# Kernel tuning notes

Hardware: AMD Instinct MI355X
Metric: run time of the kernel (lower is better)

The kernel has to match this reference:

```python
import jax, jax.numpy as jnp
import numpy as np

NS, NI, NC, C, E, M = 50000, 20000, 1000, 128, 1000000, 250000


def setup_inputs() -> dict:
    key = jax.random.key(0)
    ks = jax.random.split(key, 12)
    xavier = (2.0 / (C + C)) ** 0.5  # xavier_normal_ std for square weight
    return {
        "stu_x": jax.random.normal(ks[0], (NS, C), jnp.float32),
        "item_x": jax.random.normal(ks[1], (NI, C), jnp.float32),
        "conc_x": jax.random.normal(ks[2], (NC, C), jnp.float32),
        "W_stu": jax.random.normal(ks[3], (C, C), jnp.float32) * xavier,
        "b_stu": jnp.zeros((C,), jnp.float32),
        "W_item": jax.random.normal(ks[4], (C, C), jnp.float32) * xavier,
        "b_item": jnp.zeros((C,), jnp.float32),
        "W_pred": jax.random.normal(ks[5], (1, C), jnp.float32) * ((2.0 / (1 + C)) ** 0.5),
        "b_pred": jnp.zeros((1,), jnp.float32),
        "stu_track": jax.random.randint(ks[6], (E,), 0, NS, jnp.int32),
        "item_index": jax.random.randint(ks[7], (E,), 0, NI, jnp.int32),
        "conc_index": jax.random.randint(ks[8], (E,), 0, NC, jnp.int32),
        "mean_index": jax.random.randint(ks[9], (E,), 0, M, jnp.int32),
        "num_segments": M,
    }


def _segment_mean(vals, seg_ids, num_segments):
    sums = jax.ops.segment_sum(vals, seg_ids, num_segments=num_segments)
    cnt = jax.ops.segment_sum(jnp.ones((vals.shape[0], 1), vals.dtype), seg_ids,
                              num_segments=num_segments)
    return sums / jnp.maximum(cnt, 1.0)


def reference(stu_x, item_x, conc_x, W_stu, b_stu, W_item, b_item, W_pred, b_pred,
              stu_track, item_index, conc_index, mean_index, num_segments):
    # Feature (stu): shared lin_l=lin_r; aggregate is identity -> per-edge output
    conc_s = conc_x @ W_stu.T          # [NC, C] projected source (concepts)
    stu_p = stu_x @ W_stu.T            # [NS, C] projected target (students)
    stu_feature = jax.nn.sigmoid(conc_s[conc_index] + stu_p[stu_track] + b_stu)  # [E, C]

    # Feature (item): SparseTensor(row=item, col=conc) -> x_j from conc, x_i from item
    conc_i = conc_x @ W_item.T         # [NC, C]
    item_p = item_x @ W_item.T         # [NI, C]
    item_feature = jax.nn.sigmoid(conc_i[conc_index] + item_p[item_index] + b_item)  # [E, C]

    # scatter-mean of per-edge difference over mean_index groups
    pred_input = _segment_mean(stu_feature - item_feature, mean_index, num_segments)  # [M, C]
    pred = jax.nn.sigmoid(pred_input @ W_pred.T + b_pred)  # [M, 1]
    return pred.reshape(-1)
```

## Files before the change

### kernel.cpp

```cpp
#include <hip/hip_runtime.h>

typedef unsigned short u16;
typedef unsigned int   u32;

typedef short short8 __attribute__((ext_vector_type(8)));
typedef float floatx4 __attribute__((ext_vector_type(4)));

#define CDIM 128
#define K_NEG_LOG2E -1.4426950408889634f

__device__ __forceinline__ float bf2f_lo(u32 h) {
    union { u32 u; float f; } v; v.u = h << 16; return v.f;
}
__device__ __forceinline__ float bf2f_hi(u32 h) {
    union { u32 u; float f; } v; v.u = h & 0xffff0000u; return v.f;
}
__device__ __forceinline__ u16 f2bf(float f) {
    union { float f; u32 u; } v; v.f = f;
    u32 u = v.u;
    return (u16)((u + 0x7FFFu + ((u >> 16) & 1u)) >> 16);
}
__device__ __forceinline__ float sig_pre(float y) {
    return __builtin_amdgcn_rcpf(1.0f + __builtin_amdgcn_exp2f(y));
}
__device__ __forceinline__ float sig_std(float x) {
    return __builtin_amdgcn_rcpf(1.0f + __builtin_amdgcn_exp2f(x * K_NEG_LOG2E));
}

__global__ __launch_bounds__(256) void prep_kernel(
    const float* __restrict__ Wstu, const float* __restrict__ Witem,
    u32* __restrict__ Wbf_pair, float4* __restrict__ zero4, int nZero4)
{
    const int tid = blockIdx.x * blockDim.x + threadIdx.x;
    const int stride = gridDim.x * blockDim.x;
    for (int i = tid; i < 16384; i += stride) {
        const float* W = (i & 8192) ? (Witem - 16384) : Wstu;
        const int j = i * 2;
        u32 lo = f2bf(W[j]     * K_NEG_LOG2E);
        u32 hi = f2bf(W[j + 1] * K_NEG_LOG2E);
        Wbf_pair[i] = lo | (hi << 16);
    }
    const float4 z = {0.f, 0.f, 0.f, 0.f};
    for (int i = tid; i < nZero4; i += stride) zero4[i] = z;
}

__device__ __forceinline__ void proj_tile32(
    const float* __restrict__ X, const u16* __restrict__ Wbf,
    const float* __restrict__ bias, u16* __restrict__ out,
    int nrows, int ostride, int ooff, int row0, int lane)
{
    const int m = lane & 15;
    const int g = lane >> 4;

    short8 a[2][4];
#pragma unroll
    for (int t = 0; t < 2; ++t) {
        int arow = row0 + t * 16 + m;
        if (arow >= nrows) arow = nrows - 1;
        const float* xrow = X + (size_t)arow * CDIM;
#pragma unroll
        for (int s = 0; s < 4; ++s) {
            float4 f0 = *(const float4*)(xrow + s * 32 + g * 8);
            float4 f1 = *(const float4*)(xrow + s * 32 + g * 8 + 4);
            a[t][s][0] = (short)f2bf(f0.x); a[t][s][1] = (short)f2bf(f0.y);
            a[t][s][2] = (short)f2bf(f0.z); a[t][s][3] = (short)f2bf(f0.w);
            a[t][s][4] = (short)f2bf(f1.x); a[t][s][5] = (short)f2bf(f1.y);
            a[t][s][6] = (short)f2bf(f1.z); a[t][s][7] = (short)f2bf(f1.w);
        }
    }

#pragma unroll
    for (int ct = 0; ct < 8; ++ct) {
        const u16* wrow = Wbf + (size_t)(ct * 16 + m) * CDIM;
        floatx4 acc0 = {0.f, 0.f, 0.f, 0.f};
        floatx4 acc1 = {0.f, 0.f, 0.f, 0.f};
#pragma unroll
        for (int s = 0; s < 4; ++s) {
            short8 b = *(const short8*)(wrow + s * 32 + g * 8);
            acc0 = __builtin_amdgcn_mfma_f32_16x16x32_bf16(a[0][s], b, acc0, 0, 0, 0);
            acc1 = __builtin_amdgcn_mfma_f32_16x16x32_bf16(a[1][s], b, acc1, 0, 0, 0);
        }
        const int col = ct * 16 + m;
        const float badd = bias ? bias[col] * K_NEG_LOG2E : 0.f;
#pragma unroll
        for (int i = 0; i < 4; ++i) {
            int r0 = row0 + g * 4 + i;
            if (r0 < nrows)
                out[(size_t)r0 * ostride + ooff + col] = f2bf(acc0[i] + badd);
            int r1 = r0 + 16;
            if (r1 < nrows)
                out[(size_t)r1 * ostride + ooff + col] = f2bf(acc1[i] + badd);
        }
    }
}

__global__ __launch_bounds__(256) void proj4_kernel(
    const float* __restrict__ stu_x, const float* __restrict__ item_x,
    const float* __restrict__ conc_x,
    const u16* __restrict__ Wstu_bf, const u16* __restrict__ Witem_bf,
    const float* __restrict__ b_stu, const float* __restrict__ b_item,
    u16* __restrict__ stu_p, u16* __restrict__ item_p, u16* __restrict__ conc_cat,
    int NS, int NI, int NC)
{
    const int lane = threadIdx.x & 63;
    int w = blockIdx.x * 4 + (threadIdx.x >> 6);
    const int T0 = (NS + 31) / 32, T1 = (NI + 31) / 32, T2 = (NC + 31) / 32;

    if (w < T0) { proj_tile32(stu_x, Wstu_bf, nullptr, stu_p, NS, 128, 0, w * 32, lane); return; }
    w -= T0;
    if (w < T1) { proj_tile32(item_x, Witem_bf, nullptr, item_p, NI, 128, 0, w * 32, lane); return; }
    w -= T1;
    if (w < T2) { proj_tile32(conc_x, Wstu_bf, b_stu, conc_cat, NC, 256, 0, w * 32, lane); return; }
    w -= T2;
    if (w < T2) { proj_tile32(conc_x, Witem_bf, b_item, conc_cat, NC, 256, 128, w * 32, lane); return; }
}

__global__ __launch_bounds__(256) void edge_kernel(
    const u16* __restrict__ stu_p, const u16* __restrict__ item_p,
    const u16* __restrict__ conc_cat,
    const int* __restrict__ stu_track, const int* __restrict__ item_index,
    const int* __restrict__ conc_index, const int* __restrict__ mean_index,
    const float* __restrict__ w_pred,
    float* __restrict__ sums, float* __restrict__ cnts, int E)
{
    const int lane = threadIdx.x & 63;
    const int sub  = lane & 15;
    const int g    = lane >> 4;
    const int waveId = (int)((blockIdx.x * blockDim.x + threadIdx.x) >> 6);
    const int nWaves = (int)((gridDim.x * blockDim.x) >> 6);

    const float4 wA = ((const float4*)w_pred)[sub * 2];
    const float4 wB = ((const float4*)w_pred)[sub * 2 + 1];
    const float w8[8] = {wA.x, wA.y, wA.z, wA.w, wB.x, wB.y, wB.z, wB.w};
    const u32 lane_off = (u32)sub * 16;

    const int nQuads = (E + 3) >> 2;
    int q = waveId;
    if (q >= nQuads) return;

    int e = q * 4 + g;
    int ec = (e < E) ? e : (E - 1);
    int si = stu_track[ec], ii = item_index[ec], ci = conc_index[ec], mi = mean_index[ec];
    bool live = (e < E);

    while (true) {
        const uint4 sv = *(const uint4*)((const char*)stu_p  + (((u32)si << 8) + lane_off));
        const uint4 iv = *(const uint4*)((const char*)item_p + (((u32)ii << 8) + lane_off));
        const char* cbase = (const char*)conc_cat + (((u32)ci << 9) + lane_off);
        const uint4 ca = *(const uint4*)cbase;
        const uint4 cb = *(const uint4*)(cbase + 256);

        const int qn = q + nWaves;
        const bool more = (qn < nQuads);
        int si2, ii2, ci2, mi2; bool live2 = false;
        if (more) {
            int e2 = qn * 4 + g;
            int ec2 = (e2 < E) ? e2 : (E - 1);
            si2 = stu_track[ec2]; ii2 = item_index[ec2];
            ci2 = conc_index[ec2]; mi2 = mean_index[ec2];
            live2 = (e2 < E);
        }

        const u32 su[4] = {sv.x, sv.y, sv.z, sv.w};
        const u32 iu[4] = {iv.x, iv.y, iv.z, iv.w};
        const u32 au[4] = {ca.x, ca.y, ca.z, ca.w};
        const u32 bu[4] = {cb.x, cb.y, cb.z, cb.w};

        float v = 0.f;
#pragma unroll
        for (int j = 0; j < 4; ++j) {
            const float a0 = bf2f_lo(au[j]) + bf2f_lo(su[j]);
            const float a1 = bf2f_hi(au[j]) + bf2f_hi(su[j]);
            const float b0 = bf2f_lo(bu[j]) + bf2f_lo(iu[j]);
            const float b1 = bf2f_hi(bu[j]) + bf2f_hi(iu[j]);
            v += w8[2 * j]     * (sig_pre(a0) - sig_pre(b0));
            v += w8[2 * j + 1] * (sig_pre(a1) - sig_pre(b1));
        }

        v += __shfl_xor(v, 1, 64);
        v += __shfl_xor(v, 2, 64);
        v += __shfl_xor(v, 4, 64);
        v += __shfl_xor(v, 8, 64);

        if (sub == 0 && live) {
            atomicAdd(&sums[mi], v);
            atomicAdd(&cnts[mi], 1.0f);
        }

        if (!more) break;
        q = qn; si = si2; ii = ii2; ci = ci2; mi = mi2; live = live2;
    }
}

__global__ __launch_bounds__(256) void final_kernel(
    const float* __restrict__ sums, const float* __restrict__ cnts,
    const float* __restrict__ b_pred, float* __restrict__ out, int M)
{
    const int i = blockIdx.x * blockDim.x + threadIdx.x;
    if (i < M) {
        const float mean = sums[i] / fmaxf(cnts[i], 1.0f);
        out[i] = sig_std(mean + b_pred[0]);
    }
}

extern "C" void kernel_launch(void* const* d_in, const int* in_sizes, int n_in,
                              void* d_out, int out_size, void* d_ws, size_t ws_size,
                              hipStream_t stream) {
    const float* stu_x    = (const float*)d_in[0];
    const float* item_x   = (const float*)d_in[1];
    const float* conc_x   = (const float*)d_in[2];
    const float* W_stu    = (const float*)d_in[3];
    const float* b_stu    = (const float*)d_in[4];
    const float* W_item   = (const float*)d_in[5];
    const float* b_item   = (const float*)d_in[6];
    const float* W_pred   = (const float*)d_in[7];
    const float* b_pred   = (const float*)d_in[8];
    const int* stu_track  = (const int*)d_in[9];
    const int* item_index = (const int*)d_in[10];
    const int* conc_index = (const int*)d_in[11];
    const int* mean_index = (const int*)d_in[12];

    const int NS = in_sizes[0] / CDIM;
    const int NI = in_sizes[1] / CDIM;
    const int NC = in_sizes[2] / CDIM;
    const int E  = in_sizes[9];
    const int M  = out_size;

    float* sums    = (float*)d_ws;
    float* cnts    = sums + M;
    u16* Wstu_bf   = (u16*)(cnts + M);
    u16* Witem_bf  = Wstu_bf + CDIM * CDIM;
    u16* stu_p     = Witem_bf + CDIM * CDIM;
    u16* item_p    = stu_p  + (size_t)NS * CDIM;
    u16* conc_cat  = item_p + (size_t)NI * CDIM;

    const int nZero4 = (2 * M) / 4;
    prep_kernel<<<512, 256, 0, stream>>>(W_stu, W_item, (u32*)Wstu_bf,
                                         (float4*)sums, nZero4);

    const int T0 = (NS + 31) / 32, T1 = (NI + 31) / 32, T2 = (NC + 31) / 32;
    const int totalWaves = T0 + T1 + 2 * T2;
    proj4_kernel<<<(totalWaves + 3) / 4, 256, 0, stream>>>(
        stu_x, item_x, conc_x, Wstu_bf, Witem_bf, b_stu, b_item,
        stu_p, item_p, conc_cat, NS, NI, NC);

    edge_kernel<<<4096, 256, 0, stream>>>(stu_p, item_p, conc_cat,
                                          stu_track, item_index, conc_index, mean_index,
                                          W_pred, sums, cnts, E);

    final_kernel<<<(M + 255) / 256, 256, 0, stream>>>(sums, cnts, b_pred, (float*)d_out, M);
}
```

Measured before the change: 233.5 us.

## Store exp-domain projections, pipeline edge gathers, interleave sums and counts

The projection kernel now stores exp2 of the pre-scaled logits, so the edge kernel computes the sigmoid difference as (eb-ea)/(1+ea+eb+ea*eb) with one reciprocal instead of two exp2 plus two reciprocals per element pair. The edge loop is software-pipelined so the next quad's row gathers are issued before the current quad is computed, and index loads run two iterations ahead. Sums and counts are interleaved into one array so the two atomics and the final read hit the same cache line. The exp-domain bf16 values can overflow or lose precision for large logits, and the deeper pipeline raises register pressure.

```diff
diff --git a/kernel.cpp b/kernel.cpp
--- a/kernel.cpp
+++ b/kernel.cpp
@@ -19,9 +19,6 @@
     union { float f; u32 u; } v; v.f = f;
     u32 u = v.u;
     return (u16)((u + 0x7FFFu + ((u >> 16) & 1u)) >> 16);
-}
-__device__ __forceinline__ float sig_pre(float y) {
-    return __builtin_amdgcn_rcpf(1.0f + __builtin_amdgcn_exp2f(y));
 }
 __device__ __forceinline__ float sig_std(float x) {
     return __builtin_amdgcn_rcpf(1.0f + __builtin_amdgcn_exp2f(x * K_NEG_LOG2E));
@@ -86,10 +83,12 @@
         for (int i = 0; i < 4; ++i) {
             int r0 = row0 + g * 4 + i;
             if (r0 < nrows)
-                out[(size_t)r0 * ostride + ooff + col] = f2bf(acc0[i] + badd);
+                out[(size_t)r0 * ostride + ooff + col] =
+                    f2bf(__builtin_amdgcn_exp2f(acc0[i] + badd));
             int r1 = r0 + 16;
             if (r1 < nrows)
-                out[(size_t)r1 * ostride + ooff + col] = f2bf(acc1[i] + badd);
+                out[(size_t)r1 * ostride + ooff + col] =
+                    f2bf(__builtin_amdgcn_exp2f(acc1[i] + badd));
         }
     }
 }
@@ -121,7 +120,7 @@
     const int* __restrict__ stu_track, const int* __restrict__ item_index,
     const int* __restrict__ conc_index, const int* __restrict__ mean_index,
     const float* __restrict__ w_pred,
-    float* __restrict__ sums, float* __restrict__ cnts, int E)
+    float* __restrict__ sc, int E)
 {
     const int lane = threadIdx.x & 63;
     const int sub  = lane & 15;
@@ -138,28 +137,36 @@
     int q = waveId;
     if (q >= nQuads) return;
 
-    int e = q * 4 + g;
-    int ec = (e < E) ? e : (E - 1);
-    int si = stu_track[ec], ii = item_index[ec], ci = conc_index[ec], mi = mean_index[ec];
-    bool live = (e < E);
+#define LOADIDX(qq, sN, iN, cN, mN, lN) { \
+        int e_ = (qq) * 4 + g; int ec_ = (e_ < E) ? e_ : (E - 1); \
+        lN = (e_ < E); \
+        sN = stu_track[ec_]; iN = item_index[ec_]; \
+        cN = conc_index[ec_]; mN = mean_index[ec_]; }
+
+#define GATHER(si_, ii_, ci_, sv_, iv_, ca_, cb_) { \
+        sv_ = *(const uint4*)((const char*)stu_p  + (((u32)(si_) << 8) + lane_off)); \
+        iv_ = *(const uint4*)((const char*)item_p + (((u32)(ii_) << 8) + lane_off)); \
+        const char* cp_ = (const char*)conc_cat + (((u32)(ci_) << 9) + lane_off); \
+        ca_ = *(const uint4*)cp_; cb_ = *(const uint4*)(cp_ + 256); }
+
+    int si, ii, ci, mi; bool live;
+    LOADIDX(q, si, ii, ci, mi, live);
+    uint4 sv, iv, ca, cb;
+    GATHER(si, ii, ci, sv, iv, ca, cb);
+
+    int qn = q + nWaves;
+    bool more = (qn < nQuads);
+    int si2 = 0, ii2 = 0, ci2 = 0, mi2 = 0; bool live2 = false;
+    if (more) LOADIDX(qn, si2, ii2, ci2, mi2, live2);
 
     while (true) {
-        const uint4 sv = *(const uint4*)((const char*)stu_p  + (((u32)si << 8) + lane_off));
-        const uint4 iv = *(const uint4*)((const char*)item_p + (((u32)ii << 8) + lane_off));
-        const char* cbase = (const char*)conc_cat + (((u32)ci << 9) + lane_off);
-        const uint4 ca = *(const uint4*)cbase;
-        const uint4 cb = *(const uint4*)(cbase + 256);
-
-        const int qn = q + nWaves;
-        const bool more = (qn < nQuads);
-        int si2, ii2, ci2, mi2; bool live2 = false;
-        if (more) {
-            int e2 = qn * 4 + g;
-            int ec2 = (e2 < E) ? e2 : (E - 1);
-            si2 = stu_track[ec2]; ii2 = item_index[ec2];
-            ci2 = conc_index[ec2]; mi2 = mean_index[ec2];
-            live2 = (e2 < E);
-        }
+        uint4 svN, ivN, caN, cbN;
+        if (more) GATHER(si2, ii2, ci2, svN, ivN, caN, cbN);
+
+        const int qnn = qn + nWaves;
+        const bool more2 = (qnn < nQuads);
+        int si3 = 0, ii3 = 0, ci3 = 0, mi3 = 0; bool live3 = false;
+        if (more2) LOADIDX(qnn, si3, ii3, ci3, mi3, live3);
 
         const u32 su[4] = {sv.x, sv.y, sv.z, sv.w};
         const u32 iu[4] = {iv.x, iv.y, iv.z, iv.w};
@@ -169,12 +176,14 @@
         float v = 0.f;
 #pragma unroll
         for (int j = 0; j < 4; ++j) {
-            const float a0 = bf2f_lo(au[j]) + bf2f_lo(su[j]);
-            const float a1 = bf2f_hi(au[j]) + bf2f_hi(su[j]);
-            const float b0 = bf2f_lo(bu[j]) + bf2f_lo(iu[j]);
-            const float b1 = bf2f_hi(bu[j]) + bf2f_hi(iu[j]);
-            v += w8[2 * j]     * (sig_pre(a0) - sig_pre(b0));
-            v += w8[2 * j + 1] * (sig_pre(a1) - sig_pre(b1));
+            const float ea0 = bf2f_lo(au[j]) * bf2f_lo(su[j]);
+            const float eb0 = bf2f_lo(bu[j]) * bf2f_lo(iu[j]);
+            const float ea1 = bf2f_hi(au[j]) * bf2f_hi(su[j]);
+            const float eb1 = bf2f_hi(bu[j]) * bf2f_hi(iu[j]);
+            const float den0 = 1.0f + fmaf(ea0, eb0, ea0 + eb0);
+            const float den1 = 1.0f + fmaf(ea1, eb1, ea1 + eb1);
+            v += w8[2 * j]     * ((eb0 - ea0) * __builtin_amdgcn_rcpf(den0));
+            v += w8[2 * j + 1] * ((eb1 - ea1) * __builtin_amdgcn_rcpf(den1));
         }
 
         v += __shfl_xor(v, 1, 64);
@@ -183,22 +192,29 @@
         v += __shfl_xor(v, 8, 64);
 
         if (sub == 0 && live) {
-            atomicAdd(&sums[mi], v);
-            atomicAdd(&cnts[mi], 1.0f);
+            atomicAdd(&sc[2 * (size_t)mi], v);
+            atomicAdd(&sc[2 * (size_t)mi + 1], 1.0f);
         }
 
         if (!more) break;
-        q = qn; si = si2; ii = ii2; ci = ci2; mi = mi2; live = live2;
-    }
+        sv = svN; iv = ivN; ca = caN; cb = cbN;
+        mi = mi2; live = live2;
+        q = qn; qn = qnn;
+        si2 = si3; ii2 = ii3; ci2 = ci3; mi2 = mi3; live2 = live3;
+        more = more2;
+    }
+#undef LOADIDX
+#undef GATHER
 }
 
 __global__ __launch_bounds__(256) void final_kernel(
-    const float* __restrict__ sums, const float* __restrict__ cnts,
+    const float* __restrict__ sc,
     const float* __restrict__ b_pred, float* __restrict__ out, int M)
 {
     const int i = blockIdx.x * blockDim.x + threadIdx.x;
     if (i < M) {
-        const float mean = sums[i] / fmaxf(cnts[i], 1.0f);
+        const float2 p = ((const float2*)sc)[i];
+        const float mean = p.x / fmaxf(p.y, 1.0f);
         out[i] = sig_std(mean + b_pred[0]);
     }
 }
@@ -226,9 +242,8 @@
     const int E  = in_sizes[9];
     const int M  = out_size;
 
-    float* sums    = (float*)d_ws;
-    float* cnts    = sums + M;
-    u16* Wstu_bf   = (u16*)(cnts + M);
+    float* sc      = (float*)d_ws;
+    u16* Wstu_bf   = (u16*)(sc + 2 * (size_t)M);
     u16* Witem_bf  = Wstu_bf + CDIM * CDIM;
     u16* stu_p     = Witem_bf + CDIM * CDIM;
     u16* item_p    = stu_p  + (size_t)NS * CDIM;
@@ -236,7 +251,7 @@
 
     const int nZero4 = (2 * M) / 4;
     prep_kernel<<<512, 256, 0, stream>>>(W_stu, W_item, (u32*)Wstu_bf,
-                                         (float4*)sums, nZero4);
+                                         (float4*)sc, nZero4);
 
     const int T0 = (NS + 31) / 32, T1 = (NI + 31) / 32, T2 = (NC + 31) / 32;
     const int totalWaves = T0 + T1 + 2 * T2;
@@ -246,7 +261,7 @@
 
     edge_kernel<<<4096, 256, 0, stream>>>(stu_p, item_p, conc_cat,
                                           stu_track, item_index, conc_index, mean_index,
-                                          W_pred, sums, cnts, E);
-
-    final_kernel<<<(M + 255) / 256, 256, 0, stream>>>(sums, cnts, b_pred, (float*)d_out, M);
-}
+                                          W_pred, sc, E);
+
+    final_kernel<<<(M + 255) / 256, 256, 0, stream>>>(sc, b_pred, (float*)d_out, M);
+}
```

After: 236.0 us. No clear change (+1.1%).
